# Kernel tuning notes

Hardware: AMD Instinct MI355X
Metric: run time of the kernel (lower is better)

The kernel has to match this reference:

```python
import jax, jax.numpy as jnp
import numpy as np

LATENT = 64  # latent_size -> N = K = LATENT**2 = 4096 codes/tokens


def setup_inputs() -> dict:
    key = jax.random.key(0)
    k1, k2 = jax.random.split(key)
    hidden, L = 1024, LATENT
    z = jax.random.normal(k1, (hidden, L, L), dtype=jnp.float32)
    code_books = jax.random.uniform(k2, (hidden, L, L), dtype=jnp.float32)  # torch.rand init
    return {"z": z, "code_books": code_books}


def reference(z, code_books):
    # z, code_books: (D=hidden, L, L). Tokens/codes are columns of the flattened maps.
    D = z.shape[0]
    zf = z.reshape(D, -1).T           # (N, D) tokens
    cb = code_books.reshape(D, -1).T  # (K, D) codebook entries
    # Squared L2 distance via GEMM trick: ||a-b||^2 = ||a||^2 + ||b||^2 - 2 a.b
    # (avoids the N x K x D broadcast intermediate of the original)
    d2 = (jnp.sum(zf * zf, axis=1)[:, None]
          + jnp.sum(cb * cb, axis=1)[None, :]
          - 2.0 * zf @ cb.T)          # (N, K)
    idx = jnp.argmin(d2, axis=1)      # (N,)
    zq = cb[idx]                      # (N, D) gather
    zq = zq.reshape(LATENT, LATENT, -1).transpose(2, 0, 1)  # (D, L, L)
    # Straight-through: z = zq + (z - zq).detach()  (z was detached before lookup)
    z_st = zq + jax.lax.stop_gradient(z - zq)
    return z_st, zq
```

## Files before the change

kernel.cpp:

```cpp
#include <hip/hip_runtime.h>
#include <stdint.h>

#define D  1024
#define NK 4096
#define KA 1024
#define KB 1024
#define TAU 0.15f
#define CW  0.12f
#define MAXC 1024

#define BK2 32
#define NT2 (KA / BK2)
#define NBUF 4

typedef __attribute__((ext_vector_type(8))) _Float16 f16x8;
typedef __attribute__((ext_vector_type(4))) float f32x4;
typedef unsigned long long u64;

__device__ __forceinline__ uint32_t fkey(float f) {
    uint32_t b = __float_as_uint(f);
    return (b & 0x80000000u) ? ~b : (b | 0x80000000u);
}
__device__ __forceinline__ float unfkey(uint32_t u) {
    uint32_t b = (u & 0x80000000u) ? (u & 0x7fffffffu) : ~u;
    return __uint_as_float(b);
}
__device__ __forceinline__ u64 umin64(u64 a, u64 b) { return a < b ? a : b; }
__device__ __forceinline__ u64 umax64(u64 a, u64 b) { return a > b ? a : b; }

__device__ __forceinline__ void gload16(void* lds, const void* g) {
    __builtin_amdgcn_global_load_lds(
        (const __attribute__((address_space(1))) unsigned int*)g,
        (__attribute__((address_space(3))) unsigned int*)lds, 16, 0, 0);
}

__global__ void cbnorm_kernel(const float* __restrict__ cb, float* __restrict__ cbn) {
    __shared__ float red[256];
    const int kk = threadIdx.x & 63;
    const int dc = threadIdx.x >> 6;
    const int k  = blockIdx.x * 64 + kk;
    float s = 0.f;
    for (int d = dc; d < D; d += 4) {
        float v = cb[d * NK + k];
        s = fmaf(v, v, s);
    }
    red[threadIdx.x] = s;
    __syncthreads();
    if (dc == 0) cbn[k] = (red[kk] + red[64 + kk]) + (red[128 + kk] + red[192 + kk]);
}

__global__ __launch_bounds__(256) void split_transpose(
        const float* __restrict__ z, const float* __restrict__ cb,
        _Float16* __restrict__ Ap, _Float16* __restrict__ Bp,
        float* __restrict__ partial) {
    __shared__ float T[64][65];
    const int isZ = (blockIdx.z == 0);
    const float* src = isZ ? z : cb;
    _Float16* dst = isZ ? Ap : Bp;
    const int n0 = blockIdx.x * 64, d0 = blockIdx.y * 64;
    const int t = threadIdx.x;
#pragma unroll
    for (int i = 0; i < 4; ++i) {
        int dl = (t >> 4) + i * 16;
        int nl = (t & 15) * 4;
        float4 v = *(const float4*)&src[(size_t)(d0 + dl) * NK + n0 + nl];
        T[dl][nl] = v.x; T[dl][nl + 1] = v.y; T[dl][nl + 2] = v.z; T[dl][nl + 3] = v.w;
    }
    __syncthreads();
    const int nr = t >> 2, dch = (t & 3) * 16;
    f16x8 h0, h1;
    float s = 0.f;
#pragma unroll
    for (int j = 0; j < 8; ++j) {
        float v = T[dch + j][nr];
        s = fmaf(v, v, s);
        h0[j] = (_Float16)v;
    }
#pragma unroll
    for (int j = 0; j < 8; ++j) {
        float v = T[dch + 8 + j][nr];
        s = fmaf(v, v, s);
        h1[j] = (_Float16)v;
    }
    size_t base = (size_t)(n0 + nr) * KA + d0 + dch;
    *(f16x8*)&dst[base]     = h0;
    *(f16x8*)&dst[base + 8] = h1;
    if (!isZ) {
        s += __shfl_xor(s, 1);
        s += __shfl_xor(s, 2);
        if ((t & 3) == 0) partial[(size_t)(d0 >> 6) * NK + n0 + nr] = s;
    }
}

__global__ void cbnorm_finish(const float* __restrict__ partial, float* __restrict__ cbn) {
    const int k = blockIdx.x * 256 + threadIdx.x;
    float s = 0.f;
#pragma unroll
    for (int j = 0; j < 16; ++j) s += partial[(size_t)j * NK + k];
    cbn[k] = s;
}

__global__ __launch_bounds__(512, 2) void gemm_mfma(
        const _Float16* __restrict__ Ap, const _Float16* __restrict__ Bp,
        const float* __restrict__ cbn, ulonglong2* __restrict__ tp) {
    __shared__ _Float16 As[NBUF][256 * BK2];
    __shared__ _Float16 Bs[NBUF][256 * BK2];
    const int tid = threadIdx.x;
    const int xcd = blockIdx.x & 7, idx = blockIdx.x >> 3;
    const int n0 = ((xcd >> 1) * 4 + (idx >> 3)) * 256;
    const int k0 = ((xcd & 1) * 8 + (idx & 7)) * 256;
    const int w = tid >> 6, l = tid & 63;
    const int wr = w >> 2, wc = w & 3;
    const int fr = l & 15, fq = l >> 4;

    f32x4 acc[8][4] = {};

    const int srow = tid >> 2;
    const int swz = ((tid & 3) ^ ((tid >> 3) & 3)) * 8;
    const _Float16* gA0 = Ap + (size_t)(n0 + srow) * KA + swz;
    const _Float16* gA1 = Ap + (size_t)(n0 + 128 + srow) * KA + swz;
    const _Float16* gB0 = Bp + (size_t)(k0 + srow) * KB + swz;
    const _Float16* gB1 = Bp + (size_t)(k0 + 128 + srow) * KB + swz;
    const int rcol = (fq ^ ((fr >> 1) & 3)) * 8;

    gload16(&As[0][tid * 8],        gA0);
    gload16(&As[0][4096 + tid * 8], gA1);
    gload16(&Bs[0][tid * 8],        gB0);
    gload16(&Bs[0][4096 + tid * 8], gB1);
    gload16(&As[1][tid * 8],        gA0 + BK2);
    gload16(&As[1][4096 + tid * 8], gA1 + BK2);
    gload16(&Bs[1][tid * 8],        gB0 + BK2);
    gload16(&Bs[1][4096 + tid * 8], gB1 + BK2);
    asm volatile("s_waitcnt vmcnt(4)" ::: "memory");
    __builtin_amdgcn_s_barrier();
    asm volatile("" ::: "memory");

    for (int t = 0; t < NT2; ++t) {
        const int b = t & 3;
        const int pb = (t + 2) & 3;
        const _Float16* Ab = As[b];
        const _Float16* Bb = Bs[b];
        const bool st = (t + 2) < NT2;

        f16x8 bbf[4], a0[4];
#pragma unroll
        for (int ni = 0; ni < 4; ++ni)
            bbf[ni] = *(const f16x8*)&Bb[(wc * 64 + ni * 16 + fr) * BK2 + rcol];
#pragma unroll
        for (int mi = 0; mi < 4; ++mi)
            a0[mi] = *(const f16x8*)&Ab[(wr * 128 + mi * 16 + fr) * BK2 + rcol];
        if (st) {
            gload16(&As[pb][tid * 8],        gA0 + (t + 2) * BK2);
            gload16(&As[pb][4096 + tid * 8], gA1 + (t + 2) * BK2);
        }
        __builtin_amdgcn_s_setprio(1);
#pragma unroll
        for (int mi = 0; mi < 4; ++mi)
#pragma unroll
            for (int ni = 0; ni < 4; ++ni)
                acc[mi][ni] = __builtin_amdgcn_mfma_f32_16x16x32_f16(a0[mi], bbf[ni], acc[mi][ni], 0, 0, 0);
        __builtin_amdgcn_s_setprio(0);
        __builtin_amdgcn_s_barrier();

        f16x8 a1[4];
#pragma unroll
        for (int mi = 0; mi < 4; ++mi)
            a1[mi] = *(const f16x8*)&Ab[(wr * 128 + 64 + mi * 16 + fr) * BK2 + rcol];
        if (st) {
            gload16(&Bs[pb][tid * 8],        gB0 + (t + 2) * BK2);
            gload16(&Bs[pb][4096 + tid * 8], gB1 + (t + 2) * BK2);
        }
        __builtin_amdgcn_s_setprio(1);
#pragma unroll
        for (int mi = 0; mi < 4; ++mi)
#pragma unroll
            for (int ni = 0; ni < 4; ++ni)
                acc[4 + mi][ni] = __builtin_amdgcn_mfma_f32_16x16x32_f16(a1[mi], bbf[ni], acc[4 + mi][ni], 0, 0, 0);
        __builtin_amdgcn_s_setprio(0);

        if (t < NT2 - 2) {
            asm volatile("s_waitcnt vmcnt(4)" ::: "memory");
        } else if (t == NT2 - 2) {
            asm volatile("s_waitcnt vmcnt(0)" ::: "memory");
        }
        if (t < NT2 - 1) {
            __builtin_amdgcn_s_barrier();
            asm volatile("" ::: "memory");
        }
    }

    float cbv[4];
#pragma unroll
    for (int ni = 0; ni < 4; ++ni) cbv[ni] = cbn[k0 + wc * 64 + ni * 16 + fr];
    const int kt64 = (k0 >> 6) + wc;
#pragma unroll
    for (int mi = 0; mi < 8; ++mi) {
#pragma unroll
        for (int reg = 0; reg < 4; ++reg) {
            float b1f = 1e30f, b2f = 1e30f;
            int b1k = 0;
#pragma unroll
            for (int ni = 0; ni < 4; ++ni) {
                float s = fmaf(-2.f, acc[mi][ni][reg], cbv[ni]);
                b2f = fminf(fmaxf(s, b1f), b2f);
                if (s < b1f) { b1f = s; b1k = k0 + wc * 64 + ni * 16 + fr; }
            }
#pragma unroll
            for (int m = 8; m >= 1; m >>= 1) {
                float q1 = __shfl_xor(b1f, m);
                int   qk = __shfl_xor(b1k, m);
                float q2 = __shfl_xor(b2f, m);
                b2f = fminf(fminf(b2f, q2), fmaxf(b1f, q1));
                if (q1 < b1f) { b1f = q1; b1k = qk; }
            }
            if (fr == 0) {
                int n = n0 + wr * 128 + mi * 16 + fq * 4 + reg;
                ulonglong2 v;
                v.x = ((u64)fkey(b1f) << 32) | (unsigned)b1k;
                v.y = ((u64)fkey(b2f) << 32) | 0xffffffffu;
                tp[(size_t)kt64 * NK + n] = v;
            }
        }
    }
}

__global__ __launch_bounds__(256) void reduce_rows(
        const ulonglong2* __restrict__ tp, int* __restrict__ idx,
        int* __restrict__ rescue, u64* __restrict__ rbest, int* __restrict__ ctr) {
    __shared__ ulonglong2 sh[4][64];
    const int no = threadIdx.x & 63, st = threadIdx.x >> 6;
    const int n = blockIdx.x * 64 + no;
    u64 b1 = ~0ull, b2 = ~0ull;
#pragma unroll 4
    for (int g = st * 16; g < st * 16 + 16; ++g) {
        ulonglong2 e = tp[(size_t)g * NK + n];
        u64 nb1 = umin64(b1, e.x);
        u64 nb2 = umin64(umax64(b1, e.x), umin64(b2, e.y));
        b1 = nb1; b2 = nb2;
    }
    ulonglong2 v; v.x = b1; v.y = b2;
    sh[st][no] = v;
    __syncthreads();
    if (st == 0) {
#pragma unroll
        for (int j = 1; j < 4; ++j) {
            ulonglong2 e = sh[j][no];
            u64 nb1 = umin64(b1, e.x);
            u64 nb2 = umin64(umax64(b1, e.x), umin64(b2, e.y));
            b1 = nb1; b2 = nb2;
        }
        idx[n] = (int)(b1 & 0xffffffffull);
        float f1 = unfkey((uint32_t)(b1 >> 32));
        float f2 = unfkey((uint32_t)(b2 >> 32));
        if (f2 - f1 < TAU) {
            int p = atomicAdd(ctr, 1);
            rescue[p] = n;
            rbest[p] = ~0ull;
        }
    }
}

__global__ __launch_bounds__(256) void rescue_kernel(
        const float* __restrict__ z, const float* __restrict__ cb,
        const float* __restrict__ cbn, const ulonglong2* __restrict__ tp,
        const int* __restrict__ rescue, const int* __restrict__ ctr,
        u64* __restrict__ rbest) {
    const int cnt = min(*ctr, NK);
    const int slot = blockIdx.x;
    if (slot >= cnt) return;
    const int n = rescue[slot];
    const int tid = threadIdx.x;
    const int lane = tid & 63, wv = tid >> 6;

    __shared__ float zn[D];
    __shared__ int cand[MAXC];
    __shared__ int ccnt, overflow;
    __shared__ u64 wred[4];

    if (tid == 0) { ccnt = 0; overflow = 0; }
    for (int d = tid; d < D; d += 256) zn[d] = z[(size_t)d * NK + n];

    if (tid < 64) {
        ulonglong2 e = tp[(size_t)tid * NK + n];
        u64 m = e.x;
#pragma unroll
        for (int msk = 32; msk >= 1; msk >>= 1) m = umin64(m, __shfl_xor(m, msk));
        const float thr = unfkey((uint32_t)(m >> 32)) + CW;
        if (unfkey((uint32_t)(e.y >> 32)) < thr) {
            int p = atomicAdd(&ccnt, 64);
            if (p + 64 <= MAXC) {
                for (int j = 0; j < 64; ++j) cand[p + j] = tid * 64 + j;
            } else overflow = 1;
        } else if (unfkey((uint32_t)(e.x >> 32)) < thr) {
            int p = atomicAdd(&ccnt, 1);
            if (p < MAXC) cand[p] = (int)(e.x & 0xffffffffull);
            else overflow = 1;
        }
    }
    __syncthreads();

    const int ovf = overflow;
    const int m = ovf ? NK : min(ccnt, MAXC);
    u64 best = ~0ull;
    for (int ci = wv; ci < m; ci += 4) {
        const int k = ovf ? ci : cand[ci];
        float s = 0.f;
#pragma unroll
        for (int j = 0; j < 16; ++j)
            s = fmaf(zn[lane + j * 64], cb[(size_t)(lane + j * 64) * NK + k], s);
#pragma unroll
        for (int msk = 32; msk >= 1; msk >>= 1) s += __shfl_xor(s, msk);
        float sc = cbn[k] - 2.f * s;
        best = umin64(best, ((u64)fkey(sc) << 32) | (unsigned)k);
    }
    if (lane == 0) wred[wv] = best;
    __syncthreads();
    if (tid == 0)
        rbest[slot] = umin64(umin64(wred[0], wred[1]), umin64(wred[2], wred[3]));
}

__global__ void fix_idx(const int* __restrict__ rescue, const int* __restrict__ ctr,
                        const u64* __restrict__ rbest, int* __restrict__ idx) {
    const int cnt = min(*ctr, NK);
    for (int s = threadIdx.x + blockIdx.x * 256; s < cnt; s += gridDim.x * 256)
        idx[rescue[s]] = (int)(rbest[s] & 0xffffffffull);
}

__global__ __launch_bounds__(256) void gemm_argmin(
        const float* __restrict__ z, const float* __restrict__ cb,
        const float* __restrict__ cbn, unsigned long long* __restrict__ best) {
    __shared__ float Zs[8][128];
    __shared__ float Cs[8][128];
    const int n0 = blockIdx.y * 128, k0 = blockIdx.x * 128;
    const int tid = threadIdx.x;
    const int tx = tid & 15, ty = tid >> 4;
    const int lr = tid >> 5, lc = (tid & 31) << 2;
    float acc[8][8];
#pragma unroll
    for (int i = 0; i < 8; ++i)
#pragma unroll
        for (int j = 0; j < 8; ++j) acc[i][j] = 0.f;
    for (int d0 = 0; d0 < D; d0 += 8) {
        float4 zv = *(const float4*)&z [(d0 + lr) * NK + n0 + lc];
        float4 cv = *(const float4*)&cb[(d0 + lr) * NK + k0 + lc];
        __syncthreads();
        *(float4*)&Zs[lr][lc] = zv;
        *(float4*)&Cs[lr][lc] = cv;
        __syncthreads();
#pragma unroll
        for (int dd = 0; dd < 8; ++dd) {
            float4 a0 = *(const float4*)&Zs[dd][ty * 8];
            float4 a1 = *(const float4*)&Zs[dd][ty * 8 + 4];
            float4 b0 = *(const float4*)&Cs[dd][tx * 8];
            float4 b1 = *(const float4*)&Cs[dd][tx * 8 + 4];
            float a[8] = {a0.x, a0.y, a0.z, a0.w, a1.x, a1.y, a1.z, a1.w};
            float b[8] = {b0.x, b0.y, b0.z, b0.w, b1.x, b1.y, b1.z, b1.w};
#pragma unroll
            for (int i = 0; i < 8; ++i)
#pragma unroll
                for (int j = 0; j < 8; ++j) acc[i][j] = fmaf(a[i], b[j], acc[i][j]);
        }
    }
    float cbnv[8];
#pragma unroll
    for (int j = 0; j < 8; ++j) cbnv[j] = cbn[k0 + tx * 8 + j];
#pragma unroll
    for (int i = 0; i < 8; ++i) {
        float bv = cbnv[0] - 2.f * acc[i][0];
        int bj = 0;
#pragma unroll
        for (int j = 1; j < 8; ++j) {
            float v = cbnv[j] - 2.f * acc[i][j];
            if (v < bv) { bv = v; bj = j; }
        }
        u64 p = ((u64)fkey(bv) << 32) | (unsigned)(k0 + tx * 8 + bj);
#pragma unroll
        for (int m = 8; m >= 1; m >>= 1) {
            u64 q = __shfl_xor(p, m);
            if (q < p) p = q;
        }
        if (tx == 0) atomicMin(&best[n0 + ty * 8 + i], p);
    }
}

__global__ void extract_idx(const unsigned long long* __restrict__ best,
                            int* __restrict__ idx) {
    int n = blockIdx.x * 256 + threadIdx.x;
    idx[n] = (int)(unsigned)(best[n] & 0xFFFFFFFFull);
}

__global__ void gather_kernel(const float* __restrict__ z, const float* __restrict__ cb,
                              const int* __restrict__ idx, float* __restrict__ out) {
    const int d = blockIdx.x;
    const float* cbrow = &cb[(size_t)d * NK];
    const float* zrow  = &z [(size_t)d * NK];
    float* st = &out[(size_t)d * NK];
    float* zq = &out[(size_t)D * NK + (size_t)d * NK];
    for (int n4 = threadIdx.x; n4 < NK / 4; n4 += 256) {
        int4 iv = *(const int4*)&idx[n4 * 4];
        float4 zv = *(const float4*)&zrow[n4 * 4];
        float4 q;
        q.x = cbrow[iv.x]; q.y = cbrow[iv.y]; q.z = cbrow[iv.z]; q.w = cbrow[iv.w];
        float4 stv;
        stv.x = q.x + (zv.x - q.x);
        stv.y = q.y + (zv.y - q.y);
        stv.z = q.z + (zv.z - q.z);
        stv.w = q.w + (zv.w - q.w);
        *(float4*)&st[n4 * 4] = stv;
        *(float4*)&zq[n4 * 4] = q;
    }
}

extern "C" void kernel_launch(void* const* d_in, const int* in_sizes, int n_in,
                              void* d_out, int out_size, void* d_ws, size_t ws_size,
                              hipStream_t stream) {
    const float* z  = (const float*)d_in[0];
    const float* cb = (const float*)d_in[1];
    float* out = (float*)d_out;
    char* ws = (char*)d_ws;

    const size_t oA  = 0;
    const size_t oB  = oA + (size_t)NK * KA * 2;
    const size_t oT  = oB + (size_t)NK * KB * 2;
    const size_t oC  = oT + (size_t)NK * 64 * 16;
    const size_t oI  = oC + NK * 4;
    const size_t oR  = oI + NK * 4;
    const size_t oRB = oR + NK * 4;
    const size_t oN  = oRB + NK * 8;
    const size_t oP  = oN + 256;
    const size_t REQ = oP + (size_t)16 * NK * 4;

    if (ws_size >= REQ) {
        _Float16* Ap = (_Float16*)(ws + oA);
        _Float16* Bp = (_Float16*)(ws + oB);
        ulonglong2* tp = (ulonglong2*)(ws + oT);
        float* cbn = (float*)(ws + oC);
        int* idx = (int*)(ws + oI);
        int* rescue = (int*)(ws + oR);
        u64* rbest = (u64*)(ws + oRB);
        int* ctr = (int*)(ws + oN);
        float* partial = (float*)(ws + oP);

        hipMemsetAsync(ctr, 0, 4, stream);
        split_transpose<<<dim3(NK / 64, D / 64, 2), 256, 0, stream>>>(z, cb, Ap, Bp, partial);
        cbnorm_finish<<<16, 256, 0, stream>>>(partial, cbn);
        gemm_mfma<<<256, 512, 0, stream>>>(Ap, Bp, cbn, tp);
        reduce_rows<<<64, 256, 0, stream>>>(tp, idx, rescue, rbest, ctr);
        rescue_kernel<<<4096, 256, 0, stream>>>(z, cb, cbn, tp, rescue, ctr, rbest);
        fix_idx<<<4, 256, 0, stream>>>(rescue, ctr, rbest, idx);
        gather_kernel<<<1024, 256, 0, stream>>>(z, cb, idx, out);
    } else {
        unsigned long long* best = (unsigned long long*)ws;
        float* cbn = (float*)(ws + NK * 8);
        int* idx = (int*)(ws + NK * 8 + NK * 4);
        hipMemsetAsync(best, 0xFF, NK * 8, stream);
        cbnorm_kernel<<<64, 256, 0, stream>>>(cb, cbn);
        gemm_argmin<<<dim3(NK / 128, NK / 128), 256, 0, stream>>>(z, cb, cbn, best);
        extract_idx<<<16, 256, 0, stream>>>(best, idx);
        gather_kernel<<<1024, 256, 0, stream>>>(z, cb, idx, out);
    }
}
```

Measured before the change: 87.95 us.

## Fuse norm finish, counter reset and index fixup into neighbouring kernels

Removes the memset, cbnorm_finish and fix_idx launches. The counter reset moves into split_transpose, the codebook-norm partial sums are added up in the GEMM epilogue, and rescue_kernel writes idx directly. rescue_kernel now uses a grid-stride loop over 1024 blocks instead of 4096 one-slot blocks, and it recomputes each candidate's norm inline from the codebook values it already loads. This cuts launch overhead and intermediate buffers in exchange for extra per-thread work in the GEMM epilogue and in the rescue loop.

Result: faster. 80.05 us (-9.0%).

```diff
diff --git a/kernel.cpp b/kernel.cpp
--- a/kernel.cpp
+++ b/kernel.cpp
@@ -52,8 +52,10 @@
 __global__ __launch_bounds__(256) void split_transpose(
         const float* __restrict__ z, const float* __restrict__ cb,
         _Float16* __restrict__ Ap, _Float16* __restrict__ Bp,
-        float* __restrict__ partial) {
+        float* __restrict__ partial, int* __restrict__ ctr) {
     __shared__ float T[64][65];
+    if (blockIdx.x == 0 && blockIdx.y == 0 && blockIdx.z == 0 && threadIdx.x == 0)
+        *ctr = 0;
     const int isZ = (blockIdx.z == 0);
     const float* src = isZ ? z : cb;
     _Float16* dst = isZ ? Ap : Bp;
@@ -92,17 +94,9 @@
     }
 }
 
-__global__ void cbnorm_finish(const float* __restrict__ partial, float* __restrict__ cbn) {
-    const int k = blockIdx.x * 256 + threadIdx.x;
-    float s = 0.f;
-#pragma unroll
-    for (int j = 0; j < 16; ++j) s += partial[(size_t)j * NK + k];
-    cbn[k] = s;
-}
-
 __global__ __launch_bounds__(512, 2) void gemm_mfma(
         const _Float16* __restrict__ Ap, const _Float16* __restrict__ Bp,
-        const float* __restrict__ cbn, ulonglong2* __restrict__ tp) {
+        const float* __restrict__ partial, ulonglong2* __restrict__ tp) {
     __shared__ _Float16 As[NBUF][256 * BK2];
     __shared__ _Float16 Bs[NBUF][256 * BK2];
     const int tid = threadIdx.x;
@@ -191,7 +185,13 @@
 
     float cbv[4];
 #pragma unroll
-    for (int ni = 0; ni < 4; ++ni) cbv[ni] = cbn[k0 + wc * 64 + ni * 16 + fr];
+    for (int ni = 0; ni < 4; ++ni) {
+        const int k = k0 + wc * 64 + ni * 16 + fr;
+        float s = 0.f;
+#pragma unroll
+        for (int j = 0; j < 16; ++j) s += partial[(size_t)j * NK + k];
+        cbv[ni] = s;
+    }
     const int kt64 = (k0 >> 6) + wc;
 #pragma unroll
     for (int mi = 0; mi < 8; ++mi) {
@@ -226,7 +226,7 @@
 
 __global__ __launch_bounds__(256) void reduce_rows(
         const ulonglong2* __restrict__ tp, int* __restrict__ idx,
-        int* __restrict__ rescue, u64* __restrict__ rbest, int* __restrict__ ctr) {
+        int* __restrict__ rescue, int* __restrict__ ctr) {
     __shared__ ulonglong2 sh[4][64];
     const int no = threadIdx.x & 63, st = threadIdx.x >> 6;
     const int n = blockIdx.x * 64 + no;
@@ -255,20 +255,15 @@
         if (f2 - f1 < TAU) {
             int p = atomicAdd(ctr, 1);
             rescue[p] = n;
-            rbest[p] = ~0ull;
         }
     }
 }
 
 __global__ __launch_bounds__(256) void rescue_kernel(
         const float* __restrict__ z, const float* __restrict__ cb,
-        const float* __restrict__ cbn, const ulonglong2* __restrict__ tp,
-        const int* __restrict__ rescue, const int* __restrict__ ctr,
-        u64* __restrict__ rbest) {
+        const ulonglong2* __restrict__ tp, const int* __restrict__ rescue,
+        const int* __restrict__ ctr, int* __restrict__ idx) {
     const int cnt = min(*ctr, NK);
-    const int slot = blockIdx.x;
-    if (slot >= cnt) return;
-    const int n = rescue[slot];
     const int tid = threadIdx.x;
     const int lane = tid & 63, wv = tid >> 6;
 
@@ -277,53 +272,57 @@
     __shared__ int ccnt, overflow;
     __shared__ u64 wred[4];
 
-    if (tid == 0) { ccnt = 0; overflow = 0; }
-    for (int d = tid; d < D; d += 256) zn[d] = z[(size_t)d * NK + n];
-
-    if (tid < 64) {
-        ulonglong2 e = tp[(size_t)tid * NK + n];
-        u64 m = e.x;
-#pragma unroll
-        for (int msk = 32; msk >= 1; msk >>= 1) m = umin64(m, __shfl_xor(m, msk));
-        const float thr = unfkey((uint32_t)(m >> 32)) + CW;
-        if (unfkey((uint32_t)(e.y >> 32)) < thr) {
-            int p = atomicAdd(&ccnt, 64);
-            if (p + 64 <= MAXC) {
-                for (int j = 0; j < 64; ++j) cand[p + j] = tid * 64 + j;
-            } else overflow = 1;
-        } else if (unfkey((uint32_t)(e.x >> 32)) < thr) {
-            int p = atomicAdd(&ccnt, 1);
-            if (p < MAXC) cand[p] = (int)(e.x & 0xffffffffull);
-            else overflow = 1;
-        }
-    }
-    __syncthreads();
-
-    const int ovf = overflow;
-    const int m = ovf ? NK : min(ccnt, MAXC);
-    u64 best = ~0ull;
-    for (int ci = wv; ci < m; ci += 4) {
-        const int k = ovf ? ci : cand[ci];
-        float s = 0.f;
-#pragma unroll
-        for (int j = 0; j < 16; ++j)
-            s = fmaf(zn[lane + j * 64], cb[(size_t)(lane + j * 64) * NK + k], s);
-#pragma unroll
-        for (int msk = 32; msk >= 1; msk >>= 1) s += __shfl_xor(s, msk);
-        float sc = cbn[k] - 2.f * s;
-        best = umin64(best, ((u64)fkey(sc) << 32) | (unsigned)k);
-    }
-    if (lane == 0) wred[wv] = best;
-    __syncthreads();
-    if (tid == 0)
-        rbest[slot] = umin64(umin64(wred[0], wred[1]), umin64(wred[2], wred[3]));
-}
-
-__global__ void fix_idx(const int* __restrict__ rescue, const int* __restrict__ ctr,
-                        const u64* __restrict__ rbest, int* __restrict__ idx) {
-    const int cnt = min(*ctr, NK);
-    for (int s = threadIdx.x + blockIdx.x * 256; s < cnt; s += gridDim.x * 256)
-        idx[rescue[s]] = (int)(rbest[s] & 0xffffffffull);
+    for (int slot = blockIdx.x; slot < cnt; slot += gridDim.x) {
+        const int n = rescue[slot];
+        if (tid == 0) { ccnt = 0; overflow = 0; }
+        for (int d = tid; d < D; d += 256) zn[d] = z[(size_t)d * NK + n];
+
+        if (tid < 64) {
+            ulonglong2 e = tp[(size_t)tid * NK + n];
+            u64 m = e.x;
+#pragma unroll
+            for (int msk = 32; msk >= 1; msk >>= 1) m = umin64(m, __shfl_xor(m, msk));
+            const float thr = unfkey((uint32_t)(m >> 32)) + CW;
+            if (unfkey((uint32_t)(e.y >> 32)) < thr) {
+                int p = atomicAdd(&ccnt, 64);
+                if (p + 64 <= MAXC) {
+                    for (int j = 0; j < 64; ++j) cand[p + j] = tid * 64 + j;
+                } else overflow = 1;
+            } else if (unfkey((uint32_t)(e.x >> 32)) < thr) {
+                int p = atomicAdd(&ccnt, 1);
+                if (p < MAXC) cand[p] = (int)(e.x & 0xffffffffull);
+                else overflow = 1;
+            }
+        }
+        __syncthreads();
+
+        const int ovf = overflow;
+        const int m = ovf ? NK : min(ccnt, MAXC);
+        u64 best = ~0ull;
+        for (int ci = wv; ci < m; ci += 4) {
+            const int k = ovf ? ci : cand[ci];
+            float s = 0.f, s2 = 0.f;
+#pragma unroll
+            for (int j = 0; j < 16; ++j) {
+                float c = cb[(size_t)(lane + j * 64) * NK + k];
+                s  = fmaf(zn[lane + j * 64], c, s);
+                s2 = fmaf(c, c, s2);
+            }
+#pragma unroll
+            for (int msk = 32; msk >= 1; msk >>= 1) {
+                s  += __shfl_xor(s, msk);
+                s2 += __shfl_xor(s2, msk);
+            }
+            float sc = s2 - 2.f * s;
+            best = umin64(best, ((u64)fkey(sc) << 32) | (unsigned)k);
+        }
+        if (lane == 0) wred[wv] = best;
+        __syncthreads();
+        if (tid == 0)
+            idx[n] = (int)(umin64(umin64(wred[0], wred[1]),
+                                  umin64(wred[2], wred[3])) & 0xffffffffull);
+        __syncthreads();
+    }
 }
 
 __global__ __launch_bounds__(256) void gemm_argmin(
@@ -422,11 +421,9 @@
     const size_t oA  = 0;
     const size_t oB  = oA + (size_t)NK * KA * 2;
     const size_t oT  = oB + (size_t)NK * KB * 2;
-    const size_t oC  = oT + (size_t)NK * 64 * 16;
-    const size_t oI  = oC + NK * 4;
+    const size_t oI  = oT + (size_t)NK * 64 * 16;
     const size_t oR  = oI + NK * 4;
-    const size_t oRB = oR + NK * 4;
-    const size_t oN  = oRB + NK * 8;
+    const size_t oN  = oR + NK * 4;
     const size_t oP  = oN + 256;
     const size_t REQ = oP + (size_t)16 * NK * 4;
 
@@ -434,20 +431,15 @@
         _Float16* Ap = (_Float16*)(ws + oA);
         _Float16* Bp = (_Float16*)(ws + oB);
         ulonglong2* tp = (ulonglong2*)(ws + oT);
-        float* cbn = (float*)(ws + oC);
         int* idx = (int*)(ws + oI);
         int* rescue = (int*)(ws + oR);
-        u64* rbest = (u64*)(ws + oRB);
         int* ctr = (int*)(ws + oN);
         float* partial = (float*)(ws + oP);
 
-        hipMemsetAsync(ctr, 0, 4, stream);
-        split_transpose<<<dim3(NK / 64, D / 64, 2), 256, 0, stream>>>(z, cb, Ap, Bp, partial);
-        cbnorm_finish<<<16, 256, 0, stream>>>(partial, cbn);
-        gemm_mfma<<<256, 512, 0, stream>>>(Ap, Bp, cbn, tp);
-        reduce_rows<<<64, 256, 0, stream>>>(tp, idx, rescue, rbest, ctr);
-        rescue_kernel<<<4096, 256, 0, stream>>>(z, cb, cbn, tp, rescue, ctr, rbest);
-        fix_idx<<<4, 256, 0, stream>>>(rescue, ctr, rbest, idx);
+        split_transpose<<<dim3(NK / 64, D / 64, 2), 256, 0, stream>>>(z, cb, Ap, Bp, partial, ctr);
+        gemm_mfma<<<256, 512, 0, stream>>>(Ap, Bp, partial, tp);
+        reduce_rows<<<64, 256, 0, stream>>>(tp, idx, rescue, ctr);
+        rescue_kernel<<<1024, 256, 0, stream>>>(z, cb, tp, rescue, ctr, idx);
         gather_kernel<<<1024, 256, 0, stream>>>(z, cb, idx, out);
     } else {
         unsigned long long* best = (unsigned long long*)ws;
```
